# Optimization experiments

Hardware: AMD Instinct MI355X
Metric: run time of the kernel (lower is better)

Reference implementation:

```python
import jax, jax.numpy as jnp
import numpy as np

S, B, CIN, COUT, H, W, K = 4, 32, 128, 256, 16, 16, 3
D = CIN * K * K  # 1152, patch feature size = in_features
PRIOR_PREC = 1.0  # isotropic prior precision (prior_prec_full = PRIOR_PREC * I_D)
LOG_PREC_LR = 1.0


def _patches(x, k):
    # x: [N, C, H, W] -> [N, C*k*k, H, W]; channel-major patch ordering (matches torch unfold)
    pad = k // 2
    return jax.lax.conv_general_dilated_patches(
        x, (k, k), (1, 1), ((pad, pad), (pad, pad)),
        dimension_numbers=('NCHW', 'OIHW', 'NCHW'))


def setup_inputs() -> dict:
    key = jax.random.key(0)
    k1, k2, k3, k4 = jax.random.split(key, 4)
    X = jax.random.normal(k1, (S, B, CIN, H, W), jnp.float32)
    u = jax.random.normal(k2, (B, COUT, H, W), jnp.float32)
    log_prec_scaled = jax.random.normal(k3, (B,), jnp.float32)
    Z = jax.random.normal(k4, (S, COUT, D), jnp.float32)  # standard normal noise for rsample
    return {"X": X, "u": u, "log_prec_scaled": log_prec_scaled, "Z": Z}


def reference(X, u, log_prec_scaled, Z):
    Xi = X[:, :B]  # [S, B, CIN, H, W]
    sqrt_prec = jnp.exp(0.5 * LOG_PREC_LR * log_prec_scaled)[:, None, None, None]  # [B,1,1,1]
    Xil = sqrt_prec * Xi                     # [S, B, CIN, H, W]
    Yil = sqrt_prec * u                      # [B, COUT, H, W]

    # conv_mm: sufficient statistics via patch extraction
    P = _patches(Xil.reshape(S * B, CIN, H, W), K).reshape(S, B, D, H * W)
    Yf = Yil.reshape(B, COUT, H * W)
    XLX = jnp.einsum('sbdp,sbep->sde', P, P)       # [S, D, D]
    XLY = jnp.einsum('sbdp,bcp->sdc', P, Yf)       # [S, D, COUT]

    # rsample_logpq_weights
    prec = XLX + PRIOR_PREC * jnp.eye(D, dtype=XLX.dtype)   # [S, D, D]
    L = jnp.linalg.cholesky(prec)                            # [S, D, D], lower
    logdet_prec = 2.0 * jnp.sum(jnp.log(jnp.diagonal(L, axis1=-2, axis2=-1)), -1)  # [S]

    mu = jax.scipy.linalg.cho_solve((L, True), XLY)          # [S, D, COUT]
    # dW: solve L^T dW = Z (multi-RHS; L is shared across COUT)
    dW = jax.scipy.linalg.solve_triangular(L, jnp.swapaxes(Z, -1, -2), lower=True, trans='T')
    Wm = jnp.swapaxes(mu + dW, -1, -2)                       # [S, COUT, D]

    # logP: unnormalized MVN log-prob of each output neuron's weights under N(0, PRIOR_PREC^-1 I)
    logP = (0.5 * COUT * D * jnp.log(jnp.asarray(PRIOR_PREC, Wm.dtype))
            - 0.5 * PRIOR_PREC * jnp.sum(Wm * Wm, (-1, -2)))          # [S]
    logQ = -0.5 * jnp.sum(Z * Z, (-1, -2)) + 0.5 * COUT * logdet_prec  # [S]
    logpq = logP - logQ
    return Wm, logpq
```

## Files before the change

kernel.cpp:

```cpp
#include <hip/hip_runtime.h>
#include <math.h>

#define NS 4
#define NB 32
#define CIN 128
#define NCOUT 256
#define HWN 256
#define ND 1152
#define NK 8192
static const size_t D2 = (size_t)ND * ND;

typedef __attribute__((ext_vector_type(8))) short bf16x8;
typedef __attribute__((ext_vector_type(4))) float f32x4;

static __device__ inline unsigned short f2bf(float x) {
  unsigned int u = __float_as_uint(x);
  unsigned int r = (u + 0x7fffu + ((u >> 16) & 1u)) >> 16;
  return (unsigned short)r;
}
static __device__ inline float bf2f(unsigned short h) {
  return __uint_as_float(((unsigned int)h) << 16);
}
static __device__ inline float rdlane(float v, int l) {
  return __int_as_float(__builtin_amdgcn_readlane(__float_as_int(v), l));
}


__global__ void k_sqrtp(const float* __restrict__ lp, float* __restrict__ sp,
                        float* __restrict__ pp) {
  int b = threadIdx.x;
  if (b < NB) sp[b] = expf(0.5f * lp[b]);
  if (b < 8) pp[b] = 0.f;
}

__global__ __launch_bounds__(128) void k_patches(const float* __restrict__ X,
                                                 const float* __restrict__ sp,
                                                 unsigned short* __restrict__ Phi,
                                                 unsigned short* __restrict__ Plo) {
  int d = blockIdx.x, s = blockIdx.y, t = threadIdx.x;
  int c = d / 9, r = d % 9, ky = r / 3, kx = r % 3;
  int p0 = t * 2;
  int yy = (p0 >> 4) + ky - 1;
  int xx0 = (p0 & 15) + kx - 1;
  bool oky = (yy >= 0 && yy < 16);
  bool ok0 = oky && (xx0 >= 0) && (xx0 < 16);
  bool ok1 = oky && (xx0 + 1 >= 0) && (xx0 + 1 < 16);
  int xo = yy * 16 + xx0;
  size_t base = ((size_t)s * ND + d) * NK + p0;
  for (int b = 0; b < NB; ++b) {
    float sb = sp[b];
    const float* xb = X + ((size_t)(s * NB + b) * CIN + c) * HWN;
    float v0 = ok0 ? xb[xo] * sb : 0.f;
    float v1 = ok1 ? xb[xo + 1] * sb : 0.f;
    unsigned short h0 = f2bf(v0), h1 = f2bf(v1);
    unsigned short l0 = f2bf(v0 - bf2f(h0)), l1 = f2bf(v1 - bf2f(h1));
    size_t idx = base + (size_t)b * HWN;
    *(unsigned int*)(Phi + idx) = (unsigned int)h0 | ((unsigned int)h1 << 16);
    *(unsigned int*)(Plo + idx) = (unsigned int)l0 | ((unsigned int)l1 << 16);
  }
}

__global__ __launch_bounds__(128) void k_ytt(const float* __restrict__ u,
                                             const float* __restrict__ sp,
                                             unsigned short* __restrict__ Yhi,
                                             unsigned short* __restrict__ Ylo) {
  int c = blockIdx.x, t = threadIdx.x;
  int p0 = t * 2;
  for (int b = 0; b < NB; ++b) {
    float sb = sp[b];
    const float* ub = u + ((size_t)b * NCOUT + c) * HWN + p0;
    float v0 = ub[0] * sb, v1 = ub[1] * sb;
    unsigned short h0 = f2bf(v0), h1 = f2bf(v1);
    unsigned short l0 = f2bf(v0 - bf2f(h0)), l1 = f2bf(v1 - bf2f(h1));
    size_t idx = (size_t)c * NK + (size_t)b * HWN + p0;
    *(unsigned int*)(Yhi + idx) = (unsigned int)h0 | ((unsigned int)h1 << 16);
    *(unsigned int*)(Ylo + idx) = (unsigned int)l0 | ((unsigned int)l1 << 16);
  }
}

__global__ __launch_bounds__(256) void k_gemm_mfma(
    const unsigned short* __restrict__ Phi, const unsigned short* __restrict__ Plo,
    const unsigned short* __restrict__ Yhi, const unsigned short* __restrict__ Ylo,
    float* __restrict__ prec, float* __restrict__ prec2,
    float* __restrict__ XLY, float* __restrict__ XLY2) {
  int jt = blockIdx.x, it = blockIdx.y;
  int s = blockIdx.z >> 1, kp = blockIdx.z & 1;
  bool isX = (jt <= it);
  if (!isX && jt < 9) return;
  int i0 = it * 128;
  int j0;
  const unsigned short *Bh, *Bl;
  if (isX) {
    j0 = jt * 128;
    Bh = Phi + ((size_t)s * ND + j0) * NK;
    Bl = Plo + ((size_t)s * ND + j0) * NK;
  } else {
    j0 = (jt - 9) * 128;
    Bh = Yhi + (size_t)j0 * NK;
    Bl = Ylo + (size_t)j0 * NK;
  }
  const unsigned short* Ah = Phi + ((size_t)s * ND + i0) * NK;
  const unsigned short* Al = Plo + ((size_t)s * ND + i0) * NK;

  __shared__ unsigned short sAh[4096], sAl[4096], sBh[4096], sBl[4096];
  int tid = threadIdx.x, wave = tid >> 6, lane = tid & 63;
  int wr = wave >> 1, wc = wave & 1;

  f32x4 zero = {0.f, 0.f, 0.f, 0.f};
  f32x4 acc[4][4];
#pragma unroll
  for (int m = 0; m < 4; ++m)
#pragma unroll
    for (int n = 0; n < 4; ++n) acc[m][n] = zero;

  const unsigned short* srcs[4] = {Ah, Al, Bh, Bl};
  unsigned short* dsts[4] = {sAh, sAl, sBh, sBl};
  int r0l = lane >> 2;
  int ke = (lane & 3) * 8;
  int arow0 = wr * 64 + (lane & 15);
  int brow0 = wc * 64 + (lane & 15);
  int koff = (lane >> 4) * 8;

  int kbeg = kp * (NK / 2), kend = kbeg + NK / 2;
  for (int k0 = kbeg; k0 < kend; k0 += 32) {
    __syncthreads();
#pragma unroll
    for (int f = 0; f < 4; ++f) {
#pragma unroll
      for (int cc = 0; cc < 2; ++cc) {
        int c = wave * 2 + cc;
        const unsigned short* g = srcs[f] + (size_t)(c * 16 + r0l) * NK + k0 + ke;
        unsigned short* l = dsts[f] + c * 512;
        __builtin_amdgcn_global_load_lds(
            (const __attribute__((address_space(1))) void*)g,
            (__attribute__((address_space(3))) void*)l, 16, 0, 0);
      }
    }
    __syncthreads();
    bf16x8 ah[4], al[4], bh[4], bl[4];
#pragma unroll
    for (int m = 0; m < 4; ++m) {
      int off = (arow0 + m * 16) * 32 + koff;
      ah[m] = *(const bf16x8*)&sAh[off];
      al[m] = *(const bf16x8*)&sAl[off];
    }
#pragma unroll
    for (int n = 0; n < 4; ++n) {
      int off = (brow0 + n * 16) * 32 + koff;
      bh[n] = *(const bf16x8*)&sBh[off];
      bl[n] = *(const bf16x8*)&sBl[off];
    }
#pragma unroll
    for (int m = 0; m < 4; ++m)
#pragma unroll
      for (int n = 0; n < 4; ++n) {
        acc[m][n] = __builtin_amdgcn_mfma_f32_16x16x32_bf16(ah[m], bh[n], acc[m][n], 0, 0, 0);
        acc[m][n] = __builtin_amdgcn_mfma_f32_16x16x32_bf16(ah[m], bl[n], acc[m][n], 0, 0, 0);
        acc[m][n] = __builtin_amdgcn_mfma_f32_16x16x32_bf16(al[m], bh[n], acc[m][n], 0, 0, 0);
      }
  }

  if (isX) {
    float* base = (kp ? prec2 : prec) + (size_t)s * D2;
#pragma unroll
    for (int m = 0; m < 4; ++m) {
      int row = i0 + wr * 64 + m * 16 + (lane >> 4) * 4;
#pragma unroll
      for (int n = 0; n < 4; ++n) {
        int col = j0 + wc * 64 + n * 16 + (lane & 15);
        float* cp = base + (size_t)row * ND + col;
#pragma unroll
        for (int r = 0; r < 4; ++r) cp[(size_t)r * ND] = acc[m][n][r];
      }
    }
  } else {
    float* base = (kp ? XLY2 : XLY) + (size_t)s * ND * NCOUT;
#pragma unroll
    for (int m = 0; m < 4; ++m) {
      int row = i0 + wr * 64 + m * 16 + (lane >> 4) * 4;
#pragma unroll
      for (int n = 0; n < 4; ++n) {
        int col = j0 + wc * 64 + n * 16 + (lane & 15);
        float* cp = base + (size_t)row * NCOUT + col;
#pragma unroll
        for (int r = 0; r < 4; ++r) cp[(size_t)r * NCOUT] = acc[m][n][r];
      }
    }
  }
}

__global__ __launch_bounds__(256, 3) void k_chol_dag(
    float* __restrict__ L, const float* __restrict__ Lp2,
    float* __restrict__ iA64, float* __restrict__ logd,
    int* __restrict__ flags) {
  int t0 = blockIdx.x, s = blockIdx.y;
  int bi = 0;
  while ((bi + 1) * (bi + 2) / 2 <= t0) ++bi;
  int bj = t0 - bi * (bi + 1) / 2;
  int ib = bi * 64, jb = bj * 64;
  float* Ls = L + (size_t)s * D2;
  const float* Ps = Lp2 + (size_t)s * D2;
  int* fc = flags + s * 324;

  __shared__ float At[64][68];
  __shared__ float Bt[64][68];
  int tid = threadIdx.x, tx = tid & 15, ty = tid >> 4;
  int lane = tid & 63, w = tid >> 6;

  float acc[4][4];
#pragma unroll
  for (int r = 0; r < 4; ++r) {
    size_t idx = (size_t)(ib + ty * 4 + r) * ND + jb + tx * 4;
    float4 v = *(const float4*)(Ls + idx);
    float4 v2 = *(const float4*)(Ps + idx);
    acc[r][0] = v.x + v2.x; acc[r][1] = v.y + v2.y;
    acc[r][2] = v.z + v2.z; acc[r][3] = v.w + v2.w;
  }
  if (bi == bj) {
#pragma unroll
    for (int r = 0; r < 4; ++r)
#pragma unroll
      for (int e = 0; e < 4; ++e)
        if (ty * 4 + r == tx * 4 + e) acc[r][e] += 1.f;
  }

  for (int k = 0; k < bj; ++k) {
    if (tid == 0) {
      while (__hip_atomic_load(&fc[bi * 18 + k], __ATOMIC_RELAXED,
                               __HIP_MEMORY_SCOPE_AGENT) == 0)
        __builtin_amdgcn_s_sleep(2);
      while (__hip_atomic_load(&fc[bj * 18 + k], __ATOMIC_RELAXED,
                               __HIP_MEMORY_SCOPE_AGENT) == 0)
        __builtin_amdgcn_s_sleep(2);
      (void)__hip_atomic_load(&fc[bj * 18 + k], __ATOMIC_ACQUIRE,
                              __HIP_MEMORY_SCOPE_AGENT);
    }
    __syncthreads();
    int kb = k * 64;
    {
      int a2 = tid >> 2, km = (tid & 3) * 4;
#pragma unroll
      for (int m = 0; m < 4; ++m) {
        float4 v = *(const float4*)(Ls + (size_t)(ib + a2) * ND + kb + km + m * 16);
        At[km + m * 16 + 0][a2] = v.x;
        At[km + m * 16 + 1][a2] = v.y;
        At[km + m * 16 + 2][a2] = v.z;
        At[km + m * 16 + 3][a2] = v.w;
        float4 u4 = *(const float4*)(Ls + (size_t)(jb + a2) * ND + kb + km + m * 16);
        Bt[km + m * 16 + 0][a2] = u4.x;
        Bt[km + m * 16 + 1][a2] = u4.y;
        Bt[km + m * 16 + 2][a2] = u4.z;
        Bt[km + m * 16 + 3][a2] = u4.w;
      }
    }
    __syncthreads();
#pragma unroll
    for (int kc = 0; kc < 64; ++kc) {
      float4 a4 = *(const float4*)&At[kc][ty * 4];
      float4 b4 = *(const float4*)&Bt[kc][tx * 4];
      float ar[4] = {a4.x, a4.y, a4.z, a4.w};
      float br[4] = {b4.x, b4.y, b4.z, b4.w};
#pragma unroll
      for (int r = 0; r < 4; ++r)
#pragma unroll
        for (int e = 0; e < 4; ++e) acc[r][e] = fmaf(-ar[r], br[e], acc[r][e]);
    }
    __syncthreads();
  }

  if (bi == bj) {
#pragma unroll
    for (int r = 0; r < 4; ++r)
#pragma unroll
      for (int e = 0; e < 4; ++e) At[ty * 4 + r][tx * 4 + e] = acc[r][e];
    {
      int rr = tid >> 2, cb2 = (tid & 3) * 16;
#pragma unroll
      for (int m = 0; m < 16; ++m) Bt[rr][cb2 + m] = (rr == cb2 + m) ? 1.f : 0.f;
    }
    __syncthreads();
    float diagv = 1.f;
    for (int p = 0; p < 8; ++p) {
      int c0 = p * 8;
      if (w == 0) {
        float pa[8], xb[8];
#pragma unroll
        for (int e = 0; e < 8; ++e) {
          pa[e] = At[lane][c0 + e];
          xb[e] = Bt[c0 + e][lane];
        }
#pragma unroll
        for (int j = 0; j < 8; ++j) {
          float dj = rdlane(pa[j], c0 + j);
          float r0 = __builtin_amdgcn_rsqf(dj);
          r0 = r0 * (1.5f - 0.5f * dj * r0 * r0);
          pa[j] *= r0;
          float xj = xb[j] * r0;
          xb[j] = xj;
          if (lane == c0 + j) diagv = dj * r0;
#pragma unroll
          for (int e = j + 1; e < 8; ++e) {
            float sv = rdlane(pa[j], c0 + e);
            pa[e] = fmaf(-pa[j], sv, pa[e]);
            xb[e] = fmaf(-sv, xj, xb[e]);
          }
        }
#pragma unroll
        for (int e = 0; e < 8; ++e) {
          At[lane][c0 + e] = pa[e];
          Bt[c0 + e][lane] = xb[e];
        }
      }
      __syncthreads();
      if (p < 7) {
        float La[8], Xp[8];
#pragma unroll
        for (int e = 0; e < 8; ++e) {
          La[e] = At[lane][c0 + e];
          Xp[e] = Bt[c0 + e][lane];
        }
        for (int c = c0 + 8 + w; c < 64; c += 4) {
          float Lc[8];
#pragma unroll
          for (int e = 0; e < 8; ++e) Lc[e] = At[c][c0 + e];
          float v = At[lane][c], vb = Bt[c][lane];
#pragma unroll
          for (int e = 0; e < 8; ++e) {
            v = fmaf(-La[e], Lc[e], v);
            vb = fmaf(-Lc[e], Xp[e], vb);
          }
          At[lane][c] = v;
          Bt[c][lane] = vb;
        }
        __syncthreads();
      }
    }
    if (w == 0) logd[s * ND + ib + lane] = logf(diagv);
    {
      float* q = iA64 + (size_t)(s * 18 + bi) * 4096;
      int rr = tid >> 2, cb2 = (tid & 3) * 16;
#pragma unroll
      for (int m = 0; m < 4; ++m)
        *(float4*)(q + rr * 64 + cb2 + m * 4) = *(const float4*)&Bt[rr][cb2 + m * 4];
    }
    __threadfence();
    __syncthreads();
    if (tid == 0)
      __hip_atomic_store(&fc[bi * 18 + bi], 1, __ATOMIC_RELEASE,
                         __HIP_MEMORY_SCOPE_AGENT);
  } else {
#pragma unroll
    for (int r = 0; r < 4; ++r)
#pragma unroll
      for (int e = 0; e < 4; ++e) At[tx * 4 + e][ty * 4 + r] = acc[r][e];
    __syncthreads();
    if (tid == 0) {
      while (__hip_atomic_load(&fc[bj * 18 + bj], __ATOMIC_RELAXED,
                               __HIP_MEMORY_SCOPE_AGENT) == 0)
        __builtin_amdgcn_s_sleep(2);
      (void)__hip_atomic_load(&fc[bj * 18 + bj], __ATOMIC_ACQUIRE,
                              __HIP_MEMORY_SCOPE_AGENT);
    }
    __syncthreads();
    {
      const float* q = iA64 + (size_t)(s * 18 + bj) * 4096;
      int a2 = tid >> 2, km = (tid & 3) * 4;
#pragma unroll
      for (int m = 0; m < 4; ++m) {
        float4 v = *(const float4*)(q + a2 * 64 + km + m * 16);
        Bt[km + m * 16 + 0][a2] = v.x;
        Bt[km + m * 16 + 1][a2] = v.y;
        Bt[km + m * 16 + 2][a2] = v.z;
        Bt[km + m * 16 + 3][a2] = v.w;
      }
    }
    __syncthreads();
    float acc2[4][4] = {};
#pragma unroll
    for (int kc = 0; kc < 64; ++kc) {
      float4 a4 = *(const float4*)&At[kc][ty * 4];
      float4 b4 = *(const float4*)&Bt[kc][tx * 4];
      float ar[4] = {a4.x, a4.y, a4.z, a4.w};
      float br[4] = {b4.x, b4.y, b4.z, b4.w};
#pragma unroll
      for (int r = 0; r < 4; ++r)
#pragma unroll
        for (int e = 0; e < 4; ++e) acc2[r][e] = fmaf(ar[r], br[e], acc2[r][e]);
    }
#pragma unroll
    for (int r = 0; r < 4; ++r) {
      float4 v = {acc2[r][0], acc2[r][1], acc2[r][2], acc2[r][3]};
      *(float4*)(Ls + (size_t)(ib + ty * 4 + r) * ND + jb + tx * 4) = v;
    }
    __threadfence();
    __syncthreads();
    if (tid == 0)
      __hip_atomic_store(&fc[bi * 18 + bj], 1, __ATOMIC_RELEASE,
                         __HIP_MEMORY_SCOPE_AGENT);
  }
}

__global__ __launch_bounds__(256) void k_invd128(const float* __restrict__ L,
                                                 const float* __restrict__ iA64,
                                                 float* __restrict__ iD) {
  int q = blockIdx.x, s = blockIdx.y;
  int tid = threadIdx.x;
  const float* Ls = L + (size_t)s * D2;
  float* out = iD + ((size_t)(s * 9 + q)) * 16384;
  int b0 = q * 128;
  __shared__ float inv0[64][68];
  __shared__ float invCt[64][68];
  __shared__ float Bt[64][68];
  __shared__ float Tl[64][68];

  {
    const float* iA0 = iA64 + (size_t)(s * 18 + 2 * q) * 4096;
    const float* iA1 = iA0 + 4096;
    int i = tid >> 2, c4 = (tid & 3) * 16;
#pragma unroll
    for (int m = 0; m < 4; ++m) {
      float4 v0 = *(const float4*)(iA0 + i * 64 + c4 + m * 4);
      *(float4*)&inv0[i][c4 + m * 4] = v0;
      float4 v1 = *(const float4*)(iA1 + i * 64 + c4 + m * 4);
      invCt[c4 + m * 4 + 0][i] = v1.x;
      invCt[c4 + m * 4 + 1][i] = v1.y;
      invCt[c4 + m * 4 + 2][i] = v1.z;
      invCt[c4 + m * 4 + 3][i] = v1.w;
    }
    const float* src = Ls + (size_t)(b0 + 64 + i) * ND + b0 + c4;
#pragma unroll
    for (int m = 0; m < 4; ++m) {
      float4 v = *(const float4*)(src + m * 4);
      Bt[c4 + m * 4 + 0][i] = v.x;
      Bt[c4 + m * 4 + 1][i] = v.y;
      Bt[c4 + m * 4 + 2][i] = v.z;
      Bt[c4 + m * 4 + 3][i] = v.w;
    }
  }
  __syncthreads();

  int tx = tid & 15, ty = tid >> 4;
  float acc[4][4] = {};
#pragma unroll
  for (int k = 0; k < 64; ++k) {
    float a4[4], b4[4];
#pragma unroll
    for (int e = 0; e < 4; ++e) { a4[e] = Bt[k][ty * 4 + e]; b4[e] = inv0[k][tx * 4 + e]; }
#pragma unroll
    for (int r = 0; r < 4; ++r)
#pragma unroll
      for (int e = 0; e < 4; ++e) acc[r][e] = fmaf(a4[r], b4[e], acc[r][e]);
  }
#pragma unroll
  for (int r = 0; r < 4; ++r)
#pragma unroll
    for (int e = 0; e < 4; ++e) Tl[ty * 4 + r][tx * 4 + e] = acc[r][e];
  __syncthreads();
  float acc2[4][4] = {};
#pragma unroll
  for (int k = 0; k < 64; ++k) {
    float a4[4], b4[4];
#pragma unroll
    for (int e = 0; e < 4; ++e) { a4[e] = invCt[k][ty * 4 + e]; b4[e] = Tl[k][tx * 4 + e]; }
#pragma unroll
    for (int r = 0; r < 4; ++r)
#pragma unroll
      for (int e = 0; e < 4; ++e) acc2[r][e] = fmaf(a4[r], b4[e], acc2[r][e]);
  }
  {
    int rrow = tid >> 2, cc = (tid & 3) * 32;
    float* o = out + rrow * 128 + cc;
    if (cc < 64) {
#pragma unroll
      for (int m = 0; m < 8; ++m) {
        float4 v = {inv0[rrow][cc + m * 4 + 0], inv0[rrow][cc + m * 4 + 1],
                    inv0[rrow][cc + m * 4 + 2], inv0[rrow][cc + m * 4 + 3]};
        *(float4*)(o + m * 4) = v;
      }
    } else {
      float4 z = {0.f, 0.f, 0.f, 0.f};
#pragma unroll
      for (int m = 0; m < 8; ++m) *(float4*)(o + m * 4) = z;
    }
  }
#pragma unroll
  for (int r = 0; r < 4; ++r) {
    float4 v = {-acc2[r][0], -acc2[r][1], -acc2[r][2], -acc2[r][3]};
    *(float4*)(out + (size_t)(64 + ty * 4 + r) * 128 + tx * 4) = v;
  }
  {
    int i = tid >> 2, jc = (tid & 3) * 16;
#pragma unroll
    for (int m = 0; m < 4; ++m) {
      float4 v = {invCt[jc + m * 4 + 0][i], invCt[jc + m * 4 + 1][i],
                  invCt[jc + m * 4 + 2][i], invCt[jc + m * 4 + 3][i]};
      *(float4*)(out + (size_t)(64 + i) * 128 + 64 + jc + m * 4) = v;
    }
  }
}

__global__ __launch_bounds__(256) void k_solve2(
    const float* __restrict__ L, const float* __restrict__ iD,
    const float* __restrict__ B1, const float* __restrict__ B2,
    const float* __restrict__ Z, float* __restrict__ Xf, float* __restrict__ Xb,
    float* __restrict__ Wm, float* __restrict__ pp, int* __restrict__ flags) {
  int r = blockIdx.x, ct = blockIdx.y, s = blockIdx.z;
  int rb = r * 128, cb = ct * 64;
  const float* Ls = L + (size_t)s * D2;
  const float* Dq = iD + ((size_t)(s * 9 + r)) * 16384;
  float* Xfs = Xf + (size_t)s * ND * NCOUT;
  float* Xbs = Xb + (size_t)s * ND * NCOUT;
  int fbf = 1296 + (s * 4 + ct) * 9;
  int fbb = 1440 + (s * 4 + ct) * 9;

  __shared__ float sA[32][132];
  __shared__ float sB[32][68];
  __shared__ float red[8];
  int tid = threadIdx.x, tx = tid & 15, ty = tid >> 4;
  int wave = tid >> 6, lane = tid & 63;

  float acc[8][4];
#pragma unroll
  for (int ii = 0; ii < 8; ++ii) {
    size_t idx = (size_t)s * ND * NCOUT + (size_t)(rb + ty * 8 + ii) * NCOUT + cb + tx * 4;
    float4 v = *(const float4*)(B1 + idx);
    float4 v2 = *(const float4*)(B2 + idx);
    acc[ii][0] = v.x + v2.x; acc[ii][1] = v.y + v2.y;
    acc[ii][2] = v.z + v2.z; acc[ii][3] = v.w + v2.w;
  }
  for (int q = 0; q < r; ++q) {
    if (tid == 0) {
      while (__hip_atomic_load(&flags[fbf + q], __ATOMIC_RELAXED,
                               __HIP_MEMORY_SCOPE_AGENT) == 0)
        __builtin_amdgcn_s_sleep(2);
      (void)__hip_atomic_load(&flags[fbf + q], __ATOMIC_ACQUIRE,
                              __HIP_MEMORY_SCOPE_AGENT);
    }
    __syncthreads();
    int qb = q * 128;
    for (int kk = 0; kk < 4; ++kk) {
      __syncthreads();
      {
        int i = tid >> 1, kb = (tid & 1) * 16;
        const float* src = Ls + (size_t)(rb + i) * ND + qb + kk * 32 + kb;
#pragma unroll
        for (int m = 0; m < 4; ++m) {
          float4 v = *(const float4*)(src + m * 4);
          sA[kb + m * 4 + 0][i] = v.x;
          sA[kb + m * 4 + 1][i] = v.y;
          sA[kb + m * 4 + 2][i] = v.z;
          sA[kb + m * 4 + 3][i] = v.w;
        }
      }
      {
        int k = tid >> 3, jb2 = (tid & 7) * 8;
        const float* src = Xfs + (size_t)(qb + kk * 32 + k) * NCOUT + cb + jb2;
        float4 v0 = *(const float4*)src;
        float4 v1 = *(const float4*)(src + 4);
        *(float4*)&sB[k][jb2] = v0;
        *(float4*)&sB[k][jb2 + 4] = v1;
      }
      __syncthreads();
#pragma unroll
      for (int k = 0; k < 32; ++k) {
        float4 a0 = *(const float4*)&sA[k][ty * 8];
        float4 a1 = *(const float4*)&sA[k][ty * 8 + 4];
        float4 b0 = *(const float4*)&sB[k][tx * 4];
        float a[8] = {a0.x, a0.y, a0.z, a0.w, a1.x, a1.y, a1.z, a1.w};
        float b[4] = {b0.x, b0.y, b0.z, b0.w};
#pragma unroll
        for (int ii = 0; ii < 8; ++ii)
#pragma unroll
          for (int j = 0; j < 4; ++j) acc[ii][j] = fmaf(-a[ii], b[j], acc[ii][j]);
      }
    }
  }
  float acc2[8][4] = {};
  for (int kk = 0; kk < 4; ++kk) {
    __syncthreads();
    if ((ty >> 2) == kk) {
      int kloc = ty * 8 - kk * 32;
#pragma unroll
      for (int ii = 0; ii < 8; ++ii) {
        float4 v = {acc[ii][0], acc[ii][1], acc[ii][2], acc[ii][3]};
        *(float4*)&sB[kloc + ii][tx * 4] = v;
      }
    }
    {
      int i = tid >> 1, kb = (tid & 1) * 16;
      const float* src = Dq + (size_t)i * 128 + kk * 32 + kb;
#pragma unroll
      for (int m = 0; m < 4; ++m) {
        float4 v = *(const float4*)(src + m * 4);
        sA[kb + m * 4 + 0][i] = v.x;
        sA[kb + m * 4 + 1][i] = v.y;
        sA[kb + m * 4 + 2][i] = v.z;
        sA[kb + m * 4 + 3][i] = v.w;
      }
    }
    __syncthreads();
#pragma unroll
    for (int k = 0; k < 32; ++k) {
      float4 a0 = *(const float4*)&sA[k][ty * 8];
      float4 a1 = *(const float4*)&sA[k][ty * 8 + 4];
      float4 b0 = *(const float4*)&sB[k][tx * 4];
      float a[8] = {a0.x, a0.y, a0.z, a0.w, a1.x, a1.y, a1.z, a1.w};
      float b[4] = {b0.x, b0.y, b0.z, b0.w};
#pragma unroll
      for (int ii = 0; ii < 8; ++ii)
#pragma unroll
        for (int j = 0; j < 4; ++j) acc2[ii][j] = fmaf(a[ii], b[j], acc2[ii][j]);
    }
  }
#pragma unroll
  for (int ii = 0; ii < 8; ++ii) {
    float4 v = {acc2[ii][0], acc2[ii][1], acc2[ii][2], acc2[ii][3]};
    *(float4*)(Xfs + (size_t)(rb + ty * 8 + ii) * NCOUT + cb + tx * 4) = v;
  }
  __threadfence();
  __syncthreads();
  if (tid == 0)
    __hip_atomic_store(&flags[fbf + r], 1, __ATOMIC_RELEASE,
                       __HIP_MEMORY_SCOPE_AGENT);

#pragma unroll
  for (int ii = 0; ii < 8; ++ii)
#pragma unroll
    for (int j = 0; j < 4; ++j) acc[ii][j] = acc2[ii][j];

  float zp = 0.f;
  for (int kk = 0; kk < 4; ++kk) {
    __syncthreads();
    {
      int c = tid >> 2, d8 = (tid & 3) * 8;
      const float* src = Z + ((size_t)(s * NCOUT) + cb + c) * ND + rb + kk * 32 + d8;
      float4 v0 = *(const float4*)src;
      float4 v1 = *(const float4*)(src + 4);
      sA[d8 + 0][c] = v0.x; sA[d8 + 1][c] = v0.y; sA[d8 + 2][c] = v0.z; sA[d8 + 3][c] = v0.w;
      sA[d8 + 4][c] = v1.x; sA[d8 + 5][c] = v1.y; sA[d8 + 6][c] = v1.z; sA[d8 + 7][c] = v1.w;
      zp += v0.x * v0.x + v0.y * v0.y + v0.z * v0.z + v0.w * v0.w;
      zp += v1.x * v1.x + v1.y * v1.y + v1.z * v1.z + v1.w * v1.w;
    }
    __syncthreads();
    if ((ty >> 2) == kk) {
      int kloc = ty * 8 - kk * 32;
#pragma unroll
      for (int ii = 0; ii < 8; ++ii) {
        float4 v = *(const float4*)&sA[kloc + ii][tx * 4];
        acc[ii][0] += v.x; acc[ii][1] += v.y; acc[ii][2] += v.z; acc[ii][3] += v.w;
      }
    }
  }
#pragma unroll
  for (int m2 = 32; m2 >= 1; m2 >>= 1) zp += __shfl_xor(zp, m2, 64);
  if (lane == 0) red[wave] = zp;
  __syncthreads();
  if (tid == 0) atomicAdd(pp + s, red[0] + red[1] + red[2] + red[3]);

  for (int q = 8; q > r; --q) {
    if (tid == 0) {
      while (__hip_atomic_load(&flags[fbb + q], __ATOMIC_RELAXED,
                               __HIP_MEMORY_SCOPE_AGENT) == 0)
        __builtin_amdgcn_s_sleep(2);
      (void)__hip_atomic_load(&flags[fbb + q], __ATOMIC_ACQUIRE,
                              __HIP_MEMORY_SCOPE_AGENT);
    }
    __syncthreads();
    int qb = q * 128;
    for (int kk = 0; kk < 4; ++kk) {
      __syncthreads();
      {
        int k = tid >> 3, ib2 = (tid & 7) * 16;
        const float* src = Ls + (size_t)(qb + kk * 32 + k) * ND + rb + ib2;
#pragma unroll
        for (int m = 0; m < 4; ++m)
          *(float4*)&sA[k][ib2 + m * 4] = *(const float4*)(src + m * 4);
      }
      {
        int k = tid >> 3, jb2 = (tid & 7) * 8;
        const float* src = Xbs + (size_t)(qb + kk * 32 + k) * NCOUT + cb + jb2;
        float4 v0 = *(const float4*)src;
        float4 v1 = *(const float4*)(src + 4);
        *(float4*)&sB[k][jb2] = v0;
        *(float4*)&sB[k][jb2 + 4] = v1;
      }
      __syncthreads();
#pragma unroll
      for (int k = 0; k < 32; ++k) {
        float4 a0 = *(const float4*)&sA[k][ty * 8];
        float4 a1 = *(const float4*)&sA[k][ty * 8 + 4];
        float4 b0 = *(const float4*)&sB[k][tx * 4];
        float a[8] = {a0.x, a0.y, a0.z, a0.w, a1.x, a1.y, a1.z, a1.w};
        float b[4] = {b0.x, b0.y, b0.z, b0.w};
#pragma unroll
        for (int ii = 0; ii < 8; ++ii)
#pragma unroll
          for (int j = 0; j < 4; ++j) acc[ii][j] = fmaf(-a[ii], b[j], acc[ii][j]);
      }
    }
  }
#pragma unroll
  for (int ii = 0; ii < 8; ++ii)
#pragma unroll
    for (int j = 0; j < 4; ++j) acc2[ii][j] = 0.f;
  for (int kk = 0; kk < 4; ++kk) {
    __syncthreads();
    if ((ty >> 2) == kk) {
      int kloc = ty * 8 - kk * 32;
#pragma unroll
      for (int ii = 0; ii < 8; ++ii) {
        float4 v = {acc[ii][0], acc[ii][1], acc[ii][2], acc[ii][3]};
        *(float4*)&sB[kloc + ii][tx * 4] = v;
      }
    }
    {
      int k = tid >> 3, ib2 = (tid & 7) * 16;
      const float* src = Dq + (size_t)(kk * 32 + k) * 128 + ib2;
#pragma unroll
      for (int m = 0; m < 4; ++m)
        *(float4*)&sA[k][ib2 + m * 4] = *(const float4*)(src + m * 4);
    }
    __syncthreads();
#pragma unroll
    for (int k = 0; k < 32; ++k) {
      float4 a0 = *(const float4*)&sA[k][ty * 8];
      float4 a1 = *(const float4*)&sA[k][ty * 8 + 4];
      float4 b0 = *(const float4*)&sB[k][tx * 4];
      float a[8] = {a0.x, a0.y, a0.z, a0.w, a1.x, a1.y, a1.z, a1.w};
      float b[4] = {b0.x, b0.y, b0.z, b0.w};
#pragma unroll
      for (int ii = 0; ii < 8; ++ii)
#pragma unroll
        for (int j = 0; j < 4; ++j) acc2[ii][j] = fmaf(a[ii], b[j], acc2[ii][j]);
    }
  }
#pragma unroll
  for (int ii = 0; ii < 8; ++ii) {
    float4 v = {acc2[ii][0], acc2[ii][1], acc2[ii][2], acc2[ii][3]};
    *(float4*)(Xbs + (size_t)(rb + ty * 8 + ii) * NCOUT + cb + tx * 4) = v;
  }
  __threadfence();
  __syncthreads();
  if (tid == 0)
    __hip_atomic_store(&flags[fbb + r], 1, __ATOMIC_RELEASE,
                       __HIP_MEMORY_SCOPE_AGENT);
  float wp = 0.f;
#pragma unroll
  for (int ii = 0; ii < 8; ++ii)
#pragma unroll
    for (int j = 0; j < 4; ++j) wp += acc2[ii][j] * acc2[ii][j];
#pragma unroll
  for (int m2 = 32; m2 >= 1; m2 >>= 1) wp += __shfl_xor(wp, m2, 64);
  __syncthreads();
  if (lane == 0) red[wave] = wp;
  __syncthreads();
  if (tid == 0) atomicAdd(pp + 4 + s, red[0] + red[1] + red[2] + red[3]);
  for (int kk = 0; kk < 4; ++kk) {
    __syncthreads();
    if ((ty >> 2) == kk) {
      int kloc = ty * 8 - kk * 32;
#pragma unroll
      for (int ii = 0; ii < 8; ++ii) {
        float4 v = {acc2[ii][0], acc2[ii][1], acc2[ii][2], acc2[ii][3]};
        *(float4*)&sB[kloc + ii][tx * 4] = v;
      }
    }
    __syncthreads();
    {
      int c = tid >> 2, d8 = (tid & 3) * 8;
      float t0 = sB[d8 + 0][c], t1 = sB[d8 + 1][c], t2 = sB[d8 + 2][c], t3 = sB[d8 + 3][c];
      float t4 = sB[d8 + 4][c], t5 = sB[d8 + 5][c], t6 = sB[d8 + 6][c], t7 = sB[d8 + 7][c];
      float* dst = Wm + ((size_t)(s * NCOUT) + cb + c) * ND + rb + kk * 32 + d8;
      float4 w0 = {t0, t1, t2, t3}, w1 = {t4, t5, t6, t7};
      *(float4*)dst = w0;
      *(float4*)(dst + 4) = w1;
    }
  }
}

__global__ __launch_bounds__(256) void k_finalize(const float* __restrict__ logd,
                                                  const float* __restrict__ pp,
                                                  float* __restrict__ out) {
  int s = blockIdx.x, tid = threadIdx.x;
  __shared__ float r0[256];
  float l = 0.f;
  for (int i = tid; i < ND; i += 256) l += logd[s * ND + i];
  r0[tid] = l;
  __syncthreads();
  for (int off = 128; off; off >>= 1) {
    if (tid < off) r0[tid] += r0[tid + off];
    __syncthreads();
  }
  if (tid == 0) {
    float logdet = 2.0f * r0[0];
    out[s] = 0.5f * (pp[s] - pp[4 + s]) - 128.0f * logdet;
  }
}

extern "C" void kernel_launch(void* const* d_in, const int* in_sizes, int n_in,
                              void* d_out, int out_size, void* d_ws, size_t ws_size,
                              hipStream_t stream) {
  const float* X = (const float*)d_in[0];
  const float* u = (const float*)d_in[1];
  const float* lp = (const float*)d_in[2];
  const float* Z = (const float*)d_in[3];
  float* out = (float*)d_out;

  float* ws = (float*)d_ws;
  float* sp    = ws;
  float* invd  = sp + 64;
  float* logd  = invd + (size_t)NS * ND;
  float* pp    = logd + (size_t)NS * ND;
  int*   flags = (int*)(pp + 64);
  float* iD    = (float*)(flags + 2048);
  float* iA64  = iD + (size_t)NS * 9 * 16384;
  float* Xf    = iA64 + (size_t)NS * 18 * 4096;
  float* Xb    = Xf + (size_t)NS * ND * NCOUT;
  float* prec  = Xb + (size_t)NS * ND * NCOUT;
  float* prec2 = prec + (size_t)NS * D2;
  float* XLY   = prec2 + (size_t)NS * D2;
  float* XLY2  = XLY + (size_t)NS * ND * NCOUT;
  unsigned short* Phi = (unsigned short*)(XLY2 + (size_t)NS * ND * NCOUT);
  unsigned short* Plo = Phi + (size_t)NS * ND * NK;
  unsigned short* Yhi = Plo + (size_t)NS * ND * NK;
  unsigned short* Ylo = Yhi + (size_t)NCOUT * NK;

  hipMemsetAsync(flags, 0, 2048 * sizeof(int), stream);
  k_sqrtp<<<1, 64, 0, stream>>>(lp, sp, pp);
  k_patches<<<dim3(ND, NS), 128, 0, stream>>>(X, sp, Phi, Plo);
  k_ytt<<<NCOUT, 128, 0, stream>>>(u, sp, Yhi, Ylo);
  k_gemm_mfma<<<dim3(11, 9, NS * 2), 256, 0, stream>>>(Phi, Plo, Yhi, Ylo, prec,
                                                       prec2, XLY, XLY2);
  k_chol_dag<<<dim3(171, NS), 256, 0, stream>>>(prec, prec2, iA64, logd, flags);
  k_invd128<<<dim3(9, NS), 256, 0, stream>>>(prec, iA64, iD);
  k_solve2<<<dim3(9, 4, NS), 256, 0, stream>>>(prec, iD, XLY, XLY2, Z, Xf, Xb,
                                               out, pp, flags);
  k_finalize<<<NS, 256, 0, stream>>>(logd, pp, out + (size_t)NS * NCOUT * ND);
}
```

Baseline: 1.391 ms.

## Fuse Cholesky DAG, diagonal inverse and triangular solves into one flag-synchronized kernel

Merges the tiled Cholesky kernel, the 128-block diagonal-inverse kernel and the two-pass triangular solve into a single launch. Extra blocks beyond the 171 factorization tiles run the solves and poll per-tile completion flags, so solve work can start while later Cholesky tiles are still being factored. The 128x128 inverse-diagonal matmul is replaced by applying the 64x64 inverse blocks and the off-diagonal L21 block directly inside the solve. This removes two kernel boundaries and the iD intermediate, at the cost of more spin-wait polling, lower occupancy headroom with launch_bounds(256,4), and deadlock risk if solve blocks occupy CUs before the factor blocks they wait on are scheduled.

```diff
diff --git a/kernel.cpp b/kernel.cpp
--- a/kernel.cpp
+++ b/kernel.cpp
@@ -23,6 +23,10 @@
 }
 static __device__ inline float rdlane(float v, int l) {
   return __int_as_float(__builtin_amdgcn_readlane(__float_as_int(v), l));
+}
+static __device__ __forceinline__ void pollrelax(const int* f) {
+  while (__hip_atomic_load(f, __ATOMIC_RELAXED, __HIP_MEMORY_SCOPE_AGENT) == 0)
+    __builtin_amdgcn_s_sleep(2);
 }
 
 
@@ -189,335 +193,239 @@
   }
 }
 
-__global__ __launch_bounds__(256, 3) void k_chol_dag(
+
+static __device__ __forceinline__ void factor64(
+    float acc[4][4], float (*At)[68], float (*Bt)[68],
+    int tid, int lane, int w, int tx, int ty,
+    float* iA64q, float* logdq, int* flagq) {
+  __syncthreads();
+#pragma unroll
+  for (int r = 0; r < 4; ++r)
+#pragma unroll
+    for (int e = 0; e < 4; ++e) At[ty * 4 + r][tx * 4 + e] = acc[r][e];
+  {
+    int rr = tid >> 2, cb2 = (tid & 3) * 16;
+#pragma unroll
+    for (int m = 0; m < 16; ++m) Bt[rr][cb2 + m] = (rr == cb2 + m) ? 1.f : 0.f;
+  }
+  __syncthreads();
+  float diagv = 1.f;
+  for (int p = 0; p < 8; ++p) {
+    int c0 = p * 8;
+    if (w == 0) {
+      float pa[8], xb[8];
+#pragma unroll
+      for (int e = 0; e < 8; ++e) {
+        pa[e] = At[lane][c0 + e];
+        xb[e] = Bt[c0 + e][lane];
+      }
+#pragma unroll
+      for (int j = 0; j < 8; ++j) {
+        float dj = rdlane(pa[j], c0 + j);
+        float r0 = __builtin_amdgcn_rsqf(dj);
+        r0 = r0 * (1.5f - 0.5f * dj * r0 * r0);
+        pa[j] *= r0;
+        float xj = xb[j] * r0;
+        xb[j] = xj;
+        if (lane == c0 + j) diagv = dj * r0;
+#pragma unroll
+        for (int e = j + 1; e < 8; ++e) {
+          float sv = rdlane(pa[j], c0 + e);
+          pa[e] = fmaf(-pa[j], sv, pa[e]);
+          xb[e] = fmaf(-sv, xj, xb[e]);
+        }
+      }
+#pragma unroll
+      for (int e = 0; e < 8; ++e) {
+        At[lane][c0 + e] = pa[e];
+        Bt[c0 + e][lane] = xb[e];
+      }
+    }
+    __syncthreads();
+    if (p < 7) {
+      float La[8], Xp[8];
+#pragma unroll
+      for (int e = 0; e < 8; ++e) {
+        La[e] = At[lane][c0 + e];
+        Xp[e] = Bt[c0 + e][lane];
+      }
+      for (int c = c0 + 8 + w; c < 64; c += 4) {
+        float Lc[8];
+#pragma unroll
+        for (int e = 0; e < 8; ++e) Lc[e] = At[c][c0 + e];
+        float v = At[lane][c], vb = Bt[c][lane];
+#pragma unroll
+        for (int e = 0; e < 8; ++e) {
+          v = fmaf(-La[e], Lc[e], v);
+          vb = fmaf(-Lc[e], Xp[e], vb);
+        }
+        At[lane][c] = v;
+        Bt[c][lane] = vb;
+      }
+      __syncthreads();
+    }
+  }
+  if (w == 0) logdq[lane] = logf(diagv);
+  {
+    int rr = tid >> 2, cb2 = (tid & 3) * 16;
+#pragma unroll
+    for (int m = 0; m < 4; ++m)
+      *(float4*)(iA64q + rr * 64 + cb2 + m * 4) = *(const float4*)&Bt[rr][cb2 + m * 4];
+  }
+  __threadfence();
+  __syncthreads();
+  if (tid == 0)
+    __hip_atomic_store(flagq, 1, __ATOMIC_RELEASE, __HIP_MEMORY_SCOPE_AGENT);
+}
+
+__global__ __launch_bounds__(256, 4) void k_chol_solve(
     float* __restrict__ L, const float* __restrict__ Lp2,
     float* __restrict__ iA64, float* __restrict__ logd,
-    int* __restrict__ flags) {
-  int t0 = blockIdx.x, s = blockIdx.y;
-  int bi = 0;
-  while ((bi + 1) * (bi + 2) / 2 <= t0) ++bi;
-  int bj = t0 - bi * (bi + 1) / 2;
-  int ib = bi * 64, jb = bj * 64;
-  float* Ls = L + (size_t)s * D2;
-  const float* Ps = Lp2 + (size_t)s * D2;
-  int* fc = flags + s * 324;
-
-  __shared__ float At[64][68];
-  __shared__ float Bt[64][68];
-  int tid = threadIdx.x, tx = tid & 15, ty = tid >> 4;
-  int lane = tid & 63, w = tid >> 6;
-
-  float acc[4][4];
-#pragma unroll
-  for (int r = 0; r < 4; ++r) {
-    size_t idx = (size_t)(ib + ty * 4 + r) * ND + jb + tx * 4;
-    float4 v = *(const float4*)(Ls + idx);
-    float4 v2 = *(const float4*)(Ps + idx);
-    acc[r][0] = v.x + v2.x; acc[r][1] = v.y + v2.y;
-    acc[r][2] = v.z + v2.z; acc[r][3] = v.w + v2.w;
-  }
-  if (bi == bj) {
-#pragma unroll
-    for (int r = 0; r < 4; ++r)
-#pragma unroll
-      for (int e = 0; e < 4; ++e)
-        if (ty * 4 + r == tx * 4 + e) acc[r][e] += 1.f;
-  }
-
-  for (int k = 0; k < bj; ++k) {
-    if (tid == 0) {
-      while (__hip_atomic_load(&fc[bi * 18 + k], __ATOMIC_RELAXED,
-                               __HIP_MEMORY_SCOPE_AGENT) == 0)
-        __builtin_amdgcn_s_sleep(2);
-      while (__hip_atomic_load(&fc[bj * 18 + k], __ATOMIC_RELAXED,
-                               __HIP_MEMORY_SCOPE_AGENT) == 0)
-        __builtin_amdgcn_s_sleep(2);
-      (void)__hip_atomic_load(&fc[bj * 18 + k], __ATOMIC_ACQUIRE,
-                              __HIP_MEMORY_SCOPE_AGENT);
-    }
-    __syncthreads();
-    int kb = k * 64;
-    {
-      int a2 = tid >> 2, km = (tid & 3) * 4;
-#pragma unroll
-      for (int m = 0; m < 4; ++m) {
-        float4 v = *(const float4*)(Ls + (size_t)(ib + a2) * ND + kb + km + m * 16);
-        At[km + m * 16 + 0][a2] = v.x;
-        At[km + m * 16 + 1][a2] = v.y;
-        At[km + m * 16 + 2][a2] = v.z;
-        At[km + m * 16 + 3][a2] = v.w;
-        float4 u4 = *(const float4*)(Ls + (size_t)(jb + a2) * ND + kb + km + m * 16);
-        Bt[km + m * 16 + 0][a2] = u4.x;
-        Bt[km + m * 16 + 1][a2] = u4.y;
-        Bt[km + m * 16 + 2][a2] = u4.z;
-        Bt[km + m * 16 + 3][a2] = u4.w;
-      }
-    }
-    __syncthreads();
-#pragma unroll
-    for (int kc = 0; kc < 64; ++kc) {
-      float4 a4 = *(const float4*)&At[kc][ty * 4];
-      float4 b4 = *(const float4*)&Bt[kc][tx * 4];
-      float ar[4] = {a4.x, a4.y, a4.z, a4.w};
-      float br[4] = {b4.x, b4.y, b4.z, b4.w};
-#pragma unroll
-      for (int r = 0; r < 4; ++r)
-#pragma unroll
-        for (int e = 0; e < 4; ++e) acc[r][e] = fmaf(-ar[r], br[e], acc[r][e]);
-    }
-    __syncthreads();
-  }
-
-  if (bi == bj) {
-#pragma unroll
-    for (int r = 0; r < 4; ++r)
-#pragma unroll
-      for (int e = 0; e < 4; ++e) At[ty * 4 + r][tx * 4 + e] = acc[r][e];
-    {
-      int rr = tid >> 2, cb2 = (tid & 3) * 16;
-#pragma unroll
-      for (int m = 0; m < 16; ++m) Bt[rr][cb2 + m] = (rr == cb2 + m) ? 1.f : 0.f;
-    }
-    __syncthreads();
-    float diagv = 1.f;
-    for (int p = 0; p < 8; ++p) {
-      int c0 = p * 8;
-      if (w == 0) {
-        float pa[8], xb[8];
-#pragma unroll
-        for (int e = 0; e < 8; ++e) {
-          pa[e] = At[lane][c0 + e];
-          xb[e] = Bt[c0 + e][lane];
-        }
-#pragma unroll
-        for (int j = 0; j < 8; ++j) {
-          float dj = rdlane(pa[j], c0 + j);
-          float r0 = __builtin_amdgcn_rsqf(dj);
-          r0 = r0 * (1.5f - 0.5f * dj * r0 * r0);
-          pa[j] *= r0;
-          float xj = xb[j] * r0;
-          xb[j] = xj;
-          if (lane == c0 + j) diagv = dj * r0;
-#pragma unroll
-          for (int e = j + 1; e < 8; ++e) {
-            float sv = rdlane(pa[j], c0 + e);
-            pa[e] = fmaf(-pa[j], sv, pa[e]);
-            xb[e] = fmaf(-sv, xj, xb[e]);
-          }
-        }
-#pragma unroll
-        for (int e = 0; e < 8; ++e) {
-          At[lane][c0 + e] = pa[e];
-          Bt[c0 + e][lane] = xb[e];
-        }
-      }
-      __syncthreads();
-      if (p < 7) {
-        float La[8], Xp[8];
-#pragma unroll
-        for (int e = 0; e < 8; ++e) {
-          La[e] = At[lane][c0 + e];
-          Xp[e] = Bt[c0 + e][lane];
-        }
-        for (int c = c0 + 8 + w; c < 64; c += 4) {
-          float Lc[8];
-#pragma unroll
-          for (int e = 0; e < 8; ++e) Lc[e] = At[c][c0 + e];
-          float v = At[lane][c], vb = Bt[c][lane];
-#pragma unroll
-          for (int e = 0; e < 8; ++e) {
-            v = fmaf(-La[e], Lc[e], v);
-            vb = fmaf(-Lc[e], Xp[e], vb);
-          }
-          At[lane][c] = v;
-          Bt[c][lane] = vb;
-        }
-        __syncthreads();
-      }
-    }
-    if (w == 0) logd[s * ND + ib + lane] = logf(diagv);
-    {
-      float* q = iA64 + (size_t)(s * 18 + bi) * 4096;
-      int rr = tid >> 2, cb2 = (tid & 3) * 16;
-#pragma unroll
-      for (int m = 0; m < 4; ++m)
-        *(float4*)(q + rr * 64 + cb2 + m * 4) = *(const float4*)&Bt[rr][cb2 + m * 4];
-    }
-    __threadfence();
-    __syncthreads();
-    if (tid == 0)
-      __hip_atomic_store(&fc[bi * 18 + bi], 1, __ATOMIC_RELEASE,
-                         __HIP_MEMORY_SCOPE_AGENT);
-  } else {
-#pragma unroll
-    for (int r = 0; r < 4; ++r)
-#pragma unroll
-      for (int e = 0; e < 4; ++e) At[tx * 4 + e][ty * 4 + r] = acc[r][e];
-    __syncthreads();
-    if (tid == 0) {
-      while (__hip_atomic_load(&fc[bj * 18 + bj], __ATOMIC_RELAXED,
-                               __HIP_MEMORY_SCOPE_AGENT) == 0)
-        __builtin_amdgcn_s_sleep(2);
-      (void)__hip_atomic_load(&fc[bj * 18 + bj], __ATOMIC_ACQUIRE,
-                              __HIP_MEMORY_SCOPE_AGENT);
-    }
-    __syncthreads();
-    {
-      const float* q = iA64 + (size_t)(s * 18 + bj) * 4096;
-      int a2 = tid >> 2, km = (tid & 3) * 4;
-#pragma unroll
-      for (int m = 0; m < 4; ++m) {
-        float4 v = *(const float4*)(q + a2 * 64 + km + m * 16);
-        Bt[km + m * 16 + 0][a2] = v.x;
-        Bt[km + m * 16 + 1][a2] = v.y;
-        Bt[km + m * 16 + 2][a2] = v.z;
-        Bt[km + m * 16 + 3][a2] = v.w;
-      }
-    }
-    __syncthreads();
-    float acc2[4][4] = {};
-#pragma unroll
-    for (int kc = 0; kc < 64; ++kc) {
-      float4 a4 = *(const float4*)&At[kc][ty * 4];
-      float4 b4 = *(const float4*)&Bt[kc][tx * 4];
-      float ar[4] = {a4.x, a4.y, a4.z, a4.w};
-      float br[4] = {b4.x, b4.y, b4.z, b4.w};
-#pragma unroll
-      for (int r = 0; r < 4; ++r)
-#pragma unroll
-        for (int e = 0; e < 4; ++e) acc2[r][e] = fmaf(ar[r], br[e], acc2[r][e]);
-    }
-#pragma unroll
-    for (int r = 0; r < 4; ++r) {
-      float4 v = {acc2[r][0], acc2[r][1], acc2[r][2], acc2[r][3]};
-      *(float4*)(Ls + (size_t)(ib + ty * 4 + r) * ND + jb + tx * 4) = v;
-    }
-    __threadfence();
-    __syncthreads();
-    if (tid == 0)
-      __hip_atomic_store(&fc[bi * 18 + bj], 1, __ATOMIC_RELEASE,
-                         __HIP_MEMORY_SCOPE_AGENT);
-  }
-}
-
-__global__ __launch_bounds__(256) void k_invd128(const float* __restrict__ L,
-                                                 const float* __restrict__ iA64,
-                                                 float* __restrict__ iD) {
-  int q = blockIdx.x, s = blockIdx.y;
-  int tid = threadIdx.x;
-  const float* Ls = L + (size_t)s * D2;
-  float* out = iD + ((size_t)(s * 9 + q)) * 16384;
-  int b0 = q * 128;
-  __shared__ float inv0[64][68];
-  __shared__ float invCt[64][68];
-  __shared__ float Bt[64][68];
-  __shared__ float Tl[64][68];
-
-  {
-    const float* iA0 = iA64 + (size_t)(s * 18 + 2 * q) * 4096;
-    const float* iA1 = iA0 + 4096;
-    int i = tid >> 2, c4 = (tid & 3) * 16;
-#pragma unroll
-    for (int m = 0; m < 4; ++m) {
-      float4 v0 = *(const float4*)(iA0 + i * 64 + c4 + m * 4);
-      *(float4*)&inv0[i][c4 + m * 4] = v0;
-      float4 v1 = *(const float4*)(iA1 + i * 64 + c4 + m * 4);
-      invCt[c4 + m * 4 + 0][i] = v1.x;
-      invCt[c4 + m * 4 + 1][i] = v1.y;
-      invCt[c4 + m * 4 + 2][i] = v1.z;
-      invCt[c4 + m * 4 + 3][i] = v1.w;
-    }
-    const float* src = Ls + (size_t)(b0 + 64 + i) * ND + b0 + c4;
-#pragma unroll
-    for (int m = 0; m < 4; ++m) {
-      float4 v = *(const float4*)(src + m * 4);
-      Bt[c4 + m * 4 + 0][i] = v.x;
-      Bt[c4 + m * 4 + 1][i] = v.y;
-      Bt[c4 + m * 4 + 2][i] = v.z;
-      Bt[c4 + m * 4 + 3][i] = v.w;
-    }
-  }
-  __syncthreads();
-
-  int tx = tid & 15, ty = tid >> 4;
-  float acc[4][4] = {};
-#pragma unroll
-  for (int k = 0; k < 64; ++k) {
-    float a4[4], b4[4];
-#pragma unroll
-    for (int e = 0; e < 4; ++e) { a4[e] = Bt[k][ty * 4 + e]; b4[e] = inv0[k][tx * 4 + e]; }
-#pragma unroll
-    for (int r = 0; r < 4; ++r)
-#pragma unroll
-      for (int e = 0; e < 4; ++e) acc[r][e] = fmaf(a4[r], b4[e], acc[r][e]);
-  }
-#pragma unroll
-  for (int r = 0; r < 4; ++r)
-#pragma unroll
-    for (int e = 0; e < 4; ++e) Tl[ty * 4 + r][tx * 4 + e] = acc[r][e];
-  __syncthreads();
-  float acc2[4][4] = {};
-#pragma unroll
-  for (int k = 0; k < 64; ++k) {
-    float a4[4], b4[4];
-#pragma unroll
-    for (int e = 0; e < 4; ++e) { a4[e] = invCt[k][ty * 4 + e]; b4[e] = Tl[k][tx * 4 + e]; }
-#pragma unroll
-    for (int r = 0; r < 4; ++r)
-#pragma unroll
-      for (int e = 0; e < 4; ++e) acc2[r][e] = fmaf(a4[r], b4[e], acc2[r][e]);
-  }
-  {
-    int rrow = tid >> 2, cc = (tid & 3) * 32;
-    float* o = out + rrow * 128 + cc;
-    if (cc < 64) {
-#pragma unroll
-      for (int m = 0; m < 8; ++m) {
-        float4 v = {inv0[rrow][cc + m * 4 + 0], inv0[rrow][cc + m * 4 + 1],
-                    inv0[rrow][cc + m * 4 + 2], inv0[rrow][cc + m * 4 + 3]};
-        *(float4*)(o + m * 4) = v;
-      }
-    } else {
-      float4 z = {0.f, 0.f, 0.f, 0.f};
-#pragma unroll
-      for (int m = 0; m < 8; ++m) *(float4*)(o + m * 4) = z;
-    }
-  }
-#pragma unroll
-  for (int r = 0; r < 4; ++r) {
-    float4 v = {-acc2[r][0], -acc2[r][1], -acc2[r][2], -acc2[r][3]};
-    *(float4*)(out + (size_t)(64 + ty * 4 + r) * 128 + tx * 4) = v;
-  }
-  {
-    int i = tid >> 2, jc = (tid & 3) * 16;
-#pragma unroll
-    for (int m = 0; m < 4; ++m) {
-      float4 v = {invCt[jc + m * 4 + 0][i], invCt[jc + m * 4 + 1][i],
-                  invCt[jc + m * 4 + 2][i], invCt[jc + m * 4 + 3][i]};
-      *(float4*)(out + (size_t)(64 + i) * 128 + 64 + jc + m * 4) = v;
-    }
-  }
-}
-
-__global__ __launch_bounds__(256) void k_solve2(
-    const float* __restrict__ L, const float* __restrict__ iD,
+    int* __restrict__ flags,
     const float* __restrict__ B1, const float* __restrict__ B2,
     const float* __restrict__ Z, float* __restrict__ Xf, float* __restrict__ Xb,
-    float* __restrict__ Wm, float* __restrict__ pp, int* __restrict__ flags) {
-  int r = blockIdx.x, ct = blockIdx.y, s = blockIdx.z;
+    float* __restrict__ Wm, float* __restrict__ pp) {
+  int t0 = blockIdx.x, s = blockIdx.y;
+  __shared__ float SH[2 * 64 * 68];
+  __shared__ float red[8];
+  float (*At)[68] = (float(*)[68])SH;
+  float (*Bt)[68] = (float(*)[68])(SH + 64 * 68);
+  int tid = threadIdx.x, tx = tid & 15, ty = tid >> 4;
+  int lane = tid & 63, w = tid >> 6, wave = tid >> 6;
+  int* fc = flags + s * 324;
+
+  if (t0 < 171) {
+    int bi = 0;
+    while ((bi + 1) * (bi + 2) / 2 <= t0) ++bi;
+    int bj = t0 - bi * (bi + 1) / 2;
+    int ib = bi * 64, jb = bj * 64;
+    float* Ls = L + (size_t)s * D2;
+    const float* Ps = Lp2 + (size_t)s * D2;
+
+    float acc[4][4];
+#pragma unroll
+    for (int r = 0; r < 4; ++r) {
+      size_t idx = (size_t)(ib + ty * 4 + r) * ND + jb + tx * 4;
+      float4 v = *(const float4*)(Ls + idx);
+      float4 v2 = *(const float4*)(Ps + idx);
+      acc[r][0] = v.x + v2.x; acc[r][1] = v.y + v2.y;
+      acc[r][2] = v.z + v2.z; acc[r][3] = v.w + v2.w;
+    }
+    if (bi == bj) {
+#pragma unroll
+      for (int r = 0; r < 4; ++r)
+#pragma unroll
+        for (int e = 0; e < 4; ++e)
+          if (ty * 4 + r == tx * 4 + e) acc[r][e] += 1.f;
+    }
+
+    for (int k = 0; k < bj; ++k) {
+      if (tid == 0) {
+        pollrelax(&fc[bi * 18 + k]);
+        pollrelax(&fc[bj * 18 + k]);
+        (void)__hip_atomic_load(&fc[bj * 18 + k], __ATOMIC_ACQUIRE,
+                                __HIP_MEMORY_SCOPE_AGENT);
+      }
+      __syncthreads();
+      int kb = k * 64;
+      {
+        int a2 = tid >> 2, km = (tid & 3) * 4;
+#pragma unroll
+        for (int m = 0; m < 4; ++m) {
+          float4 v = *(const float4*)(Ls + (size_t)(ib + a2) * ND + kb + km + m * 16);
+          At[km + m * 16 + 0][a2] = v.x;
+          At[km + m * 16 + 1][a2] = v.y;
+          At[km + m * 16 + 2][a2] = v.z;
+          At[km + m * 16 + 3][a2] = v.w;
+          float4 u4 = *(const float4*)(Ls + (size_t)(jb + a2) * ND + kb + km + m * 16);
+          Bt[km + m * 16 + 0][a2] = u4.x;
+          Bt[km + m * 16 + 1][a2] = u4.y;
+          Bt[km + m * 16 + 2][a2] = u4.z;
+          Bt[km + m * 16 + 3][a2] = u4.w;
+        }
+      }
+      __syncthreads();
+#pragma unroll
+      for (int kc = 0; kc < 64; ++kc) {
+        float4 a4 = *(const float4*)&At[kc][ty * 4];
+        float4 b4 = *(const float4*)&Bt[kc][tx * 4];
+        float ar[4] = {a4.x, a4.y, a4.z, a4.w};
+        float br[4] = {b4.x, b4.y, b4.z, b4.w};
+#pragma unroll
+        for (int r = 0; r < 4; ++r)
+#pragma unroll
+          for (int e = 0; e < 4; ++e) acc[r][e] = fmaf(-ar[r], br[e], acc[r][e]);
+      }
+      __syncthreads();
+    }
+
+    if (bi == bj) {
+      factor64(acc, At, Bt, tid, lane, w, tx, ty,
+               iA64 + (size_t)(s * 18 + bi) * 4096, logd + (size_t)s * ND + ib,
+               &fc[bi * 18 + bi]);
+    } else {
+#pragma unroll
+      for (int r = 0; r < 4; ++r)
+#pragma unroll
+        for (int e = 0; e < 4; ++e) At[tx * 4 + e][ty * 4 + r] = acc[r][e];
+      if (tid == 0) {
+        pollrelax(&fc[bj * 18 + bj]);
+        (void)__hip_atomic_load(&fc[bj * 18 + bj], __ATOMIC_ACQUIRE,
+                                __HIP_MEMORY_SCOPE_AGENT);
+      }
+      __syncthreads();
+      {
+        const float* q = iA64 + (size_t)(s * 18 + bj) * 4096;
+        int a2 = tid >> 2, km = (tid & 3) * 4;
+#pragma unroll
+        for (int m = 0; m < 4; ++m) {
+          float4 v = *(const float4*)(q + a2 * 64 + km + m * 16);
+          Bt[km + m * 16 + 0][a2] = v.x;
+          Bt[km + m * 16 + 1][a2] = v.y;
+          Bt[km + m * 16 + 2][a2] = v.z;
+          Bt[km + m * 16 + 3][a2] = v.w;
+        }
+      }
+      __syncthreads();
+      float acc2[4][4] = {};
+#pragma unroll
+      for (int kc = 0; kc < 64; ++kc) {
+        float4 a4 = *(const float4*)&At[kc][ty * 4];
+        float4 b4 = *(const float4*)&Bt[kc][tx * 4];
+        float ar[4] = {a4.x, a4.y, a4.z, a4.w};
+        float br[4] = {b4.x, b4.y, b4.z, b4.w};
+#pragma unroll
+        for (int r = 0; r < 4; ++r)
+#pragma unroll
+          for (int e = 0; e < 4; ++e) acc2[r][e] = fmaf(ar[r], br[e], acc2[r][e]);
+      }
+#pragma unroll
+      for (int r = 0; r < 4; ++r) {
+        float4 v = {acc2[r][0], acc2[r][1], acc2[r][2], acc2[r][3]};
+        *(float4*)(Ls + (size_t)(ib + ty * 4 + r) * ND + jb + tx * 4) = v;
+      }
+      __threadfence();
+      __syncthreads();
+      if (tid == 0)
+        __hip_atomic_store(&fc[bi * 18 + bj], 1, __ATOMIC_RELEASE,
+                           __HIP_MEMORY_SCOPE_AGENT);
+    }
+    return;
+  }
+
+  int j0 = t0 - 171;
+  int r = j0 >> 2, ct = j0 & 3;
   int rb = r * 128, cb = ct * 64;
   const float* Ls = L + (size_t)s * D2;
-  const float* Dq = iD + ((size_t)(s * 9 + r)) * 16384;
   float* Xfs = Xf + (size_t)s * ND * NCOUT;
   float* Xbs = Xb + (size_t)s * ND * NCOUT;
   int fbf = 1296 + (s * 4 + ct) * 9;
   int fbb = 1440 + (s * 4 + ct) * 9;
-
-  __shared__ float sA[32][132];
-  __shared__ float sB[32][68];
-  __shared__ float red[8];
-  int tid = threadIdx.x, tx = tid & 15, ty = tid >> 4;
-  int wave = tid >> 6, lane = tid & 63;
+  const float* i11p = iA64 + (size_t)(s * 18 + 2 * r) * 4096;
+  const float* i22p = i11p + 4096;
+  const float* L21p = Ls + (size_t)(rb + 64) * ND + rb;
+  float (*sA)[132] = (float(*)[132])SH;
+  float (*sB)[68] = (float(*)[68])(SH + 64 * 68);
 
   float acc[8][4];
 #pragma unroll
@@ -530,9 +438,11 @@
   }
   for (int q = 0; q < r; ++q) {
     if (tid == 0) {
-      while (__hip_atomic_load(&flags[fbf + q], __ATOMIC_RELAXED,
-                               __HIP_MEMORY_SCOPE_AGENT) == 0)
-        __builtin_amdgcn_s_sleep(2);
+      pollrelax(&fc[(2 * r) * 18 + 2 * q]);
+      pollrelax(&fc[(2 * r) * 18 + 2 * q + 1]);
+      pollrelax(&fc[(2 * r + 1) * 18 + 2 * q]);
+      pollrelax(&fc[(2 * r + 1) * 18 + 2 * q + 1]);
+      pollrelax(&flags[fbf + q]);
       (void)__hip_atomic_load(&flags[fbf + q], __ATOMIC_ACQUIRE,
                               __HIP_MEMORY_SCOPE_AGENT);
     }
@@ -571,50 +481,130 @@
 #pragma unroll
         for (int ii = 0; ii < 8; ++ii)
 #pragma unroll
-          for (int j = 0; j < 4; ++j) acc[ii][j] = fmaf(-a[ii], b[j], acc[ii][j]);
-      }
-    }
-  }
-  float acc2[8][4] = {};
-  for (int kk = 0; kk < 4; ++kk) {
-    __syncthreads();
-    if ((ty >> 2) == kk) {
-      int kloc = ty * 8 - kk * 32;
+          for (int jj = 0; jj < 4; ++jj) acc[ii][jj] = fmaf(-a[ii], b[jj], acc[ii][jj]);
+      }
+    }
+  }
+  if (tid == 0) {
+    pollrelax(&fc[(2 * r) * 18 + 2 * r]);
+    pollrelax(&fc[(2 * r + 1) * 18 + 2 * r + 1]);
+    pollrelax(&fc[(2 * r + 1) * 18 + 2 * r]);
+    (void)__hip_atomic_load(&fc[(2 * r + 1) * 18 + 2 * r], __ATOMIC_ACQUIRE,
+                            __HIP_MEMORY_SCOPE_AGENT);
+  }
+  __syncthreads();
+  if (ty < 8) {
+#pragma unroll
+    for (int ii = 0; ii < 8; ++ii) {
+      float4 v = {acc[ii][0], acc[ii][1], acc[ii][2], acc[ii][3]};
+      *(float4*)&Bt[ty * 8 + ii][tx * 4] = v;
+    }
+  }
+  {
+    int a2 = tid >> 2, km = (tid & 3) * 4;
+#pragma unroll
+    for (int m = 0; m < 4; ++m) {
+      float4 v = *(const float4*)(i11p + (size_t)a2 * 64 + km + m * 16);
+      At[km + m * 16 + 0][a2] = v.x;
+      At[km + m * 16 + 1][a2] = v.y;
+      At[km + m * 16 + 2][a2] = v.z;
+      At[km + m * 16 + 3][a2] = v.w;
+    }
+  }
+  __syncthreads();
+  float xr[8][4];
+  if (ty < 8) {
+#pragma unroll
+    for (int ii = 0; ii < 8; ++ii)
+#pragma unroll
+      for (int jj = 0; jj < 4; ++jj) xr[ii][jj] = 0.f;
+#pragma unroll
+    for (int k = 0; k < 64; ++k) {
+      float4 b0 = *(const float4*)&Bt[k][tx * 4];
+      float b[4] = {b0.x, b0.y, b0.z, b0.w};
 #pragma unroll
       for (int ii = 0; ii < 8; ++ii) {
-        float4 v = {acc[ii][0], acc[ii][1], acc[ii][2], acc[ii][3]};
-        *(float4*)&sB[kloc + ii][tx * 4] = v;
-      }
-    }
-    {
-      int i = tid >> 1, kb = (tid & 1) * 16;
-      const float* src = Dq + (size_t)i * 128 + kk * 32 + kb;
-#pragma unroll
-      for (int m = 0; m < 4; ++m) {
-        float4 v = *(const float4*)(src + m * 4);
-        sA[kb + m * 4 + 0][i] = v.x;
-        sA[kb + m * 4 + 1][i] = v.y;
-        sA[kb + m * 4 + 2][i] = v.z;
-        sA[kb + m * 4 + 3][i] = v.w;
-      }
-    }
-    __syncthreads();
-#pragma unroll
-    for (int k = 0; k < 32; ++k) {
-      float4 a0 = *(const float4*)&sA[k][ty * 8];
-      float4 a1 = *(const float4*)&sA[k][ty * 8 + 4];
-      float4 b0 = *(const float4*)&sB[k][tx * 4];
-      float a[8] = {a0.x, a0.y, a0.z, a0.w, a1.x, a1.y, a1.z, a1.w};
+        float a = At[k][ty * 8 + ii];
+#pragma unroll
+        for (int jj = 0; jj < 4; ++jj) xr[ii][jj] = fmaf(a, b[jj], xr[ii][jj]);
+      }
+    }
+  }
+  __syncthreads();
+  if (ty < 8) {
+#pragma unroll
+    for (int ii = 0; ii < 8; ++ii) {
+      float4 v = {xr[ii][0], xr[ii][1], xr[ii][2], xr[ii][3]};
+      *(float4*)&Bt[ty * 8 + ii][tx * 4] = v;
+#pragma unroll
+      for (int jj = 0; jj < 4; ++jj) acc[ii][jj] = xr[ii][jj];
+    }
+  }
+  {
+    int a2 = tid >> 2, km = (tid & 3) * 4;
+#pragma unroll
+    for (int m = 0; m < 4; ++m) {
+      float4 v = *(const float4*)(L21p + (size_t)a2 * ND + km + m * 16);
+      At[km + m * 16 + 0][a2] = v.x;
+      At[km + m * 16 + 1][a2] = v.y;
+      At[km + m * 16 + 2][a2] = v.z;
+      At[km + m * 16 + 3][a2] = v.w;
+    }
+  }
+  __syncthreads();
+  if (ty >= 8) {
+#pragma unroll
+    for (int k = 0; k < 64; ++k) {
+      float4 b0 = *(const float4*)&Bt[k][tx * 4];
       float b[4] = {b0.x, b0.y, b0.z, b0.w};
 #pragma unroll
-      for (int ii = 0; ii < 8; ++ii)
-#pragma unroll
-        for (int j = 0; j < 4; ++j) acc2[ii][j] = fmaf(a[ii], b[j], acc2[ii][j]);
+      for (int ii = 0; ii < 8; ++ii) {
+        float a = At[k][(ty - 8) * 8 + ii];
+#pragma unroll
+        for (int jj = 0; jj < 4; ++jj) acc[ii][jj] = fmaf(-a, b[jj], acc[ii][jj]);
+      }
+    }
+  }
+  __syncthreads();
+  if (ty >= 8) {
+#pragma unroll
+    for (int ii = 0; ii < 8; ++ii) {
+      float4 v = {acc[ii][0], acc[ii][1], acc[ii][2], acc[ii][3]};
+      *(float4*)&Bt[(ty - 8) * 8 + ii][tx * 4] = v;
+    }
+  }
+  {
+    int a2 = tid >> 2, km = (tid & 3) * 4;
+#pragma unroll
+    for (int m = 0; m < 4; ++m) {
+      float4 v = *(const float4*)(i22p + (size_t)a2 * 64 + km + m * 16);
+      At[km + m * 16 + 0][a2] = v.x;
+      At[km + m * 16 + 1][a2] = v.y;
+      At[km + m * 16 + 2][a2] = v.z;
+      At[km + m * 16 + 3][a2] = v.w;
+    }
+  }
+  __syncthreads();
+  if (ty >= 8) {
+#pragma unroll
+    for (int ii = 0; ii < 8; ++ii)
+#pragma unroll
+      for (int jj = 0; jj < 4; ++jj) acc[ii][jj] = 0.f;
+#pragma unroll
+    for (int k = 0; k < 64; ++k) {
+      float4 b0 = *(const float4*)&Bt[k][tx * 4];
+      float b[4] = {b0.x, b0.y, b0.z, b0.w};
+#pragma unroll
+      for (int ii = 0; ii < 8; ++ii) {
+        float a = At[k][(ty - 8) * 8 + ii];
+#pragma unroll
+        for (int jj = 0; jj < 4; ++jj) acc[ii][jj] = fmaf(a, b[jj], acc[ii][jj]);
+      }
     }
   }
 #pragma unroll
   for (int ii = 0; ii < 8; ++ii) {
-    float4 v = {acc2[ii][0], acc2[ii][1], acc2[ii][2], acc2[ii][3]};
+    float4 v = {acc[ii][0], acc[ii][1], acc[ii][2], acc[ii][3]};
     *(float4*)(Xfs + (size_t)(rb + ty * 8 + ii) * NCOUT + cb + tx * 4) = v;
   }
   __threadfence();
@@ -622,11 +612,6 @@
   if (tid == 0)
     __hip_atomic_store(&flags[fbf + r], 1, __ATOMIC_RELEASE,
                        __HIP_MEMORY_SCOPE_AGENT);
-
-#pragma unroll
-  for (int ii = 0; ii < 8; ++ii)
-#pragma unroll
-    for (int j = 0; j < 4; ++j) acc[ii][j] = acc2[ii][j];
 
   float zp = 0.f;
   for (int kk = 0; kk < 4; ++kk) {
@@ -659,9 +644,11 @@
 
   for (int q = 8; q > r; --q) {
     if (tid == 0) {
-      while (__hip_atomic_load(&flags[fbb + q], __ATOMIC_RELAXED,
-                               __HIP_MEMORY_SCOPE_AGENT) == 0)
-        __builtin_amdgcn_s_sleep(2);
+      pollrelax(&fc[(2 * q) * 18 + 2 * r]);
+      pollrelax(&fc[(2 * q) * 18 + 2 * r + 1]);
+      pollrelax(&fc[(2 * q + 1) * 18 + 2 * r]);
+      pollrelax(&fc[(2 * q + 1) * 18 + 2 * r + 1]);
+      pollrelax(&flags[fbb + q]);
       (void)__hip_atomic_load(&flags[fbb + q], __ATOMIC_ACQUIRE,
                               __HIP_MEMORY_SCOPE_AGENT);
     }
@@ -695,48 +682,107 @@
 #pragma unroll
         for (int ii = 0; ii < 8; ++ii)
 #pragma unroll
-          for (int j = 0; j < 4; ++j) acc[ii][j] = fmaf(-a[ii], b[j], acc[ii][j]);
-      }
-    }
-  }
-#pragma unroll
-  for (int ii = 0; ii < 8; ++ii)
-#pragma unroll
-    for (int j = 0; j < 4; ++j) acc2[ii][j] = 0.f;
-  for (int kk = 0; kk < 4; ++kk) {
-    __syncthreads();
-    if ((ty >> 2) == kk) {
-      int kloc = ty * 8 - kk * 32;
+          for (int jj = 0; jj < 4; ++jj) acc[ii][jj] = fmaf(-a[ii], b[jj], acc[ii][jj]);
+      }
+    }
+  }
+  __syncthreads();
+  if (ty >= 8) {
+#pragma unroll
+    for (int ii = 0; ii < 8; ++ii) {
+      float4 v = {acc[ii][0], acc[ii][1], acc[ii][2], acc[ii][3]};
+      *(float4*)&Bt[(ty - 8) * 8 + ii][tx * 4] = v;
+    }
+  }
+  {
+    int rr2 = tid >> 2, c4 = (tid & 3) * 16;
+#pragma unroll
+    for (int m = 0; m < 4; ++m)
+      *(float4*)&At[rr2][c4 + m * 4] = *(const float4*)(i22p + (size_t)rr2 * 64 + c4 + m * 4);
+  }
+  __syncthreads();
+  if (ty >= 8) {
+#pragma unroll
+    for (int ii = 0; ii < 8; ++ii)
+#pragma unroll
+      for (int jj = 0; jj < 4; ++jj) xr[ii][jj] = 0.f;
+#pragma unroll
+    for (int k = 0; k < 64; ++k) {
+      float4 b0 = *(const float4*)&Bt[k][tx * 4];
+      float b[4] = {b0.x, b0.y, b0.z, b0.w};
 #pragma unroll
       for (int ii = 0; ii < 8; ++ii) {
-        float4 v = {acc[ii][0], acc[ii][1], acc[ii][2], acc[ii][3]};
-        *(float4*)&sB[kloc + ii][tx * 4] = v;
-      }
-    }
-    {
-      int k = tid >> 3, ib2 = (tid & 7) * 16;
-      const float* src = Dq + (size_t)(kk * 32 + k) * 128 + ib2;
-#pragma unroll
-      for (int m = 0; m < 4; ++m)
-        *(float4*)&sA[k][ib2 + m * 4] = *(const float4*)(src + m * 4);
-    }
-    __syncthreads();
-#pragma unroll
-    for (int k = 0; k < 32; ++k) {
-      float4 a0 = *(const float4*)&sA[k][ty * 8];
-      float4 a1 = *(const float4*)&sA[k][ty * 8 + 4];
-      float4 b0 = *(const float4*)&sB[k][tx * 4];
-      float a[8] = {a0.x, a0.y, a0.z, a0.w, a1.x, a1.y, a1.z, a1.w};
+        float a = At[k][(ty - 8) * 8 + ii];
+#pragma unroll
+        for (int jj = 0; jj < 4; ++jj) xr[ii][jj] = fmaf(a, b[jj], xr[ii][jj]);
+      }
+    }
+  }
+  __syncthreads();
+  if (ty >= 8) {
+#pragma unroll
+    for (int ii = 0; ii < 8; ++ii) {
+      float4 v = {xr[ii][0], xr[ii][1], xr[ii][2], xr[ii][3]};
+      *(float4*)&Bt[(ty - 8) * 8 + ii][tx * 4] = v;
+#pragma unroll
+      for (int jj = 0; jj < 4; ++jj) acc[ii][jj] = xr[ii][jj];
+    }
+  }
+  {
+    int rr2 = tid >> 2, c4 = (tid & 3) * 16;
+#pragma unroll
+    for (int m = 0; m < 4; ++m)
+      *(float4*)&At[rr2][c4 + m * 4] = *(const float4*)(L21p + (size_t)rr2 * ND + c4 + m * 4);
+  }
+  __syncthreads();
+  if (ty < 8) {
+#pragma unroll
+    for (int k = 0; k < 64; ++k) {
+      float4 b0 = *(const float4*)&Bt[k][tx * 4];
       float b[4] = {b0.x, b0.y, b0.z, b0.w};
 #pragma unroll
-      for (int ii = 0; ii < 8; ++ii)
-#pragma unroll
-        for (int j = 0; j < 4; ++j) acc2[ii][j] = fmaf(a[ii], b[j], acc2[ii][j]);
+      for (int ii = 0; ii < 8; ++ii) {
+        float a = At[k][ty * 8 + ii];
+#pragma unroll
+        for (int jj = 0; jj < 4; ++jj) acc[ii][jj] = fmaf(-a, b[jj], acc[ii][jj]);
+      }
+    }
+  }
+  __syncthreads();
+  if (ty < 8) {
+#pragma unroll
+    for (int ii = 0; ii < 8; ++ii) {
+      float4 v = {acc[ii][0], acc[ii][1], acc[ii][2], acc[ii][3]};
+      *(float4*)&Bt[ty * 8 + ii][tx * 4] = v;
+    }
+  }
+  {
+    int rr2 = tid >> 2, c4 = (tid & 3) * 16;
+#pragma unroll
+    for (int m = 0; m < 4; ++m)
+      *(float4*)&At[rr2][c4 + m * 4] = *(const float4*)(i11p + (size_t)rr2 * 64 + c4 + m * 4);
+  }
+  __syncthreads();
+  if (ty < 8) {
+#pragma unroll
+    for (int ii = 0; ii < 8; ++ii)
+#pragma unroll
+      for (int jj = 0; jj < 4; ++jj) acc[ii][jj] = 0.f;
+#pragma unroll
+    for (int k = 0; k < 64; ++k) {
+      float4 b0 = *(const float4*)&Bt[k][tx * 4];
+      float b[4] = {b0.x, b0.y, b0.z, b0.w};
+#pragma unroll
+      for (int ii = 0; ii < 8; ++ii) {
+        float a = At[k][ty * 8 + ii];
+#pragma unroll
+        for (int jj = 0; jj < 4; ++jj) acc[ii][jj] = fmaf(a, b[jj], acc[ii][jj]);
+      }
     }
   }
 #pragma unroll
   for (int ii = 0; ii < 8; ++ii) {
-    float4 v = {acc2[ii][0], acc2[ii][1], acc2[ii][2], acc2[ii][3]};
+    float4 v = {acc[ii][0], acc[ii][1], acc[ii][2], acc[ii][3]};
     *(float4*)(Xbs + (size_t)(rb + ty * 8 + ii) * NCOUT + cb + tx * 4) = v;
   }
   __threadfence();
@@ -748,7 +794,7 @@
 #pragma unroll
   for (int ii = 0; ii < 8; ++ii)
 #pragma unroll
-    for (int j = 0; j < 4; ++j) wp += acc2[ii][j] * acc2[ii][j];
+    for (int jj = 0; jj < 4; ++jj) wp += acc[ii][jj] * acc[ii][jj];
 #pragma unroll
   for (int m2 = 32; m2 >= 1; m2 >>= 1) wp += __shfl_xor(wp, m2, 64);
   __syncthreads();
@@ -761,17 +807,17 @@
       int kloc = ty * 8 - kk * 32;
 #pragma unroll
       for (int ii = 0; ii < 8; ++ii) {
-        float4 v = {acc2[ii][0], acc2[ii][1], acc2[ii][2], acc2[ii][3]};
+        float4 v = {acc[ii][0], acc[ii][1], acc[ii][2], acc[ii][3]};
         *(float4*)&sB[kloc + ii][tx * 4] = v;
       }
     }
     __syncthreads();
     {
       int c = tid >> 2, d8 = (tid & 3) * 8;
-      float t0 = sB[d8 + 0][c], t1 = sB[d8 + 1][c], t2 = sB[d8 + 2][c], t3 = sB[d8 + 3][c];
-      float t4 = sB[d8 + 4][c], t5 = sB[d8 + 5][c], t6 = sB[d8 + 6][c], t7 = sB[d8 + 7][c];
+      float t0v = sB[d8 + 0][c], t1v = sB[d8 + 1][c], t2v = sB[d8 + 2][c], t3v = sB[d8 + 3][c];
+      float t4v = sB[d8 + 4][c], t5v = sB[d8 + 5][c], t6v = sB[d8 + 6][c], t7v = sB[d8 + 7][c];
       float* dst = Wm + ((size_t)(s * NCOUT) + cb + c) * ND + rb + kk * 32 + d8;
-      float4 w0 = {t0, t1, t2, t3}, w1 = {t4, t5, t6, t7};
+      float4 w0 = {t0v, t1v, t2v, t3v}, w1 = {t4v, t5v, t6v, t7v};
       *(float4*)dst = w0;
       *(float4*)(dst + 4) = w1;
     }
@@ -831,9 +877,7 @@
   k_ytt<<<NCOUT, 128, 0, stream>>>(u, sp, Yhi, Ylo);
   k_gemm_mfma<<<dim3(11, 9, NS * 2), 256, 0, stream>>>(Phi, Plo, Yhi, Ylo, prec,
                                                        prec2, XLY, XLY2);
-  k_chol_dag<<<dim3(171, NS), 256, 0, stream>>>(prec, prec2, iA64, logd, flags);
-  k_invd128<<<dim3(9, NS), 256, 0, stream>>>(prec, iA64, iD);
-  k_solve2<<<dim3(9, 4, NS), 256, 0, stream>>>(prec, iD, XLY, XLY2, Z, Xf, Xb,
-                                               out, pp, flags);
+  k_chol_solve<<<dim3(171 + 36, NS), 256, 0, stream>>>(
+      prec, prec2, iA64, logd, flags, XLY, XLY2, Z, Xf, Xb, out, pp);
   k_finalize<<<NS, 256, 0, stream>>>(logd, pp, out + (size_t)NS * NCOUT * ND);
 }
```

Measured after the change: 1.565 ms. 12.5% more time.
